# Kernel tuning notes

Measured on AMD Instinct MI355X. Metric: run time of the kernel, lower is better.

Reference implementation:

```python
import jax, jax.numpy as jnp
import numpy as np

B, H, S, DH = 1, 16, 4096, 64
SPARSITY = 0.1
NEG = -1e9


def setup_inputs() -> dict:
    key = jax.random.key(0)
    kq, kk, kv, kp, km = jax.random.split(key, 5)
    query = jax.random.normal(kq, (B, H, S, DH), dtype=jnp.float32)
    k_ = jax.random.normal(kk, (B, H, S, DH), dtype=jnp.float32)
    v_ = jax.random.normal(kv, (B, H, S, DH), dtype=jnp.float32)
    pat = jax.random.uniform(kp, (S, S)) < SPARSITY
    pat = pat | jnp.eye(S, dtype=bool)
    sparse_pattern = pat[None, None]  # [1,1,S,S]
    mask = jax.random.randint(km, (1, 1, 1, S), 0, 2, dtype=jnp.int32)
    return {"query": query, "key": k_, "value": v_,
            "sparse_pattern": sparse_pattern, "mask": mask}


def reference(query, key, value, sparse_pattern, mask):
    scale = 1.0 / jnp.sqrt(jnp.asarray(DH, dtype=query.dtype))
    # [B,H,S,S] attention scores
    scores = jnp.einsum('bhqd,bhkd->bhqk', query, key) * scale
    scores = jnp.where(sparse_pattern, scores, NEG)
    scores = jnp.where(mask == 0, NEG, scores)
    weights = jax.nn.softmax(scores, axis=-1)
    return jnp.einsum('bhqk,bhkd->bhqd', weights, value)
```

## Files before the change

### kernel.cpp

```cpp
#include <hip/hip_runtime.h>
#include <hip/hip_bf16.h>

#define S_LEN 4096
#define DHD   64
#define NH    16
#define NKT   64
#define KVB   64
#define WQ    32
#define NW    4
#define QB    (WQ * NW)
#define QSCALE 0.18033688011112042f
#define THRS   8.656170245333781f

#if __has_builtin(__builtin_amdgcn_exp2f)
#define EXP2(x) __builtin_amdgcn_exp2f(x)
#else
#define EXP2(x) exp2f(x)
#endif

typedef __bf16 bf16x8 __attribute__((ext_vector_type(8)));
typedef __bf16 bf16x4 __attribute__((ext_vector_type(4)));
typedef float  f32x16 __attribute__((ext_vector_type(16)));
typedef float  f32x4  __attribute__((ext_vector_type(4)));
typedef unsigned u32;
typedef unsigned u32x4v __attribute__((ext_vector_type(4)));
typedef unsigned long long u64;

__device__ __forceinline__ int swz(int row, int col) {
  return row * 64 + ((((col >> 3) ^ (row & 7)) << 3) | (col & 7));
}

__device__ __forceinline__ u32 pk(float a, float b) {
  __bf16 x = (__bf16)a, y = (__bf16)b;
  u32 lo = (u32)__builtin_bit_cast(unsigned short, x);
  u32 hi = (u32)__builtin_bit_cast(unsigned short, y);
  return lo | (hi << 16);
}

__device__ __forceinline__ void gload16(const void* g, void* l) {
  __builtin_amdgcn_global_load_lds((const __attribute__((address_space(1))) void*)g,
                                   (__attribute__((address_space(3))) void*)l, 16, 0, 0);
}

__device__ __forceinline__ void plswap(u32& x, u32& y) {
  asm("v_permlane32_swap_b32 %0, %1" : "+v"(x), "+v"(y));
}

union PAW { u32x4v w; bf16x8 h; };

template <int MODE>
__device__ __forceinline__ bool patget(const void* __restrict__ p, int q, int k) {
  const size_t idx = (size_t)q * S_LEN + k;
  if constexpr (MODE == 1) return ((const unsigned char*)p)[idx] != 0;
  else if constexpr (MODE == 0) return ((const int*)p)[idx] != 0;
  else return ((const float*)p)[idx] != 0.0f;
}

__global__ void __launch_bounds__(256, 2) attn32c(
    const float* __restrict__ Qg, const __bf16* __restrict__ Kc, const __bf16* __restrict__ Vc,
    const u64* __restrict__ packw,
    const int* __restrict__ cntp, float* __restrict__ out) {
  __shared__ __align__(16) __bf16 Kls[2][KVB * DHD];
  __shared__ __align__(16) __bf16 Vls[2][DHD * KVB];
  __shared__ float sfb[NW][WQ];

  const int gid = (blockIdx.x & 7) * 64 + (blockIdx.x >> 3);
  const int h = gid >> 5;
  const int q0 = (gid & 31) * QB;

  const int t = threadIdx.x, lane = t & 63, wv = t >> 6;
  const int l32 = lane & 31, hi = lane >> 5;
  const int qrow = q0 + wv * WQ + l32;
  const int nact = cntp[0];
  const int nt = (nact + 63) >> 6;

  bf16x8 aQ[4];
  {
    const float* qp = Qg + ((size_t)h * S_LEN + qrow) * DHD;
#pragma unroll
    for (int c = 0; c < 4; c++) {
      float4 x = *(const float4*)(qp + c * 16 + hi * 8);
      float4 y = *(const float4*)(qp + c * 16 + hi * 8 + 4);
      bf16x8 f;
      f[0] = (__bf16)(x.x * QSCALE); f[1] = (__bf16)(x.y * QSCALE);
      f[2] = (__bf16)(x.z * QSCALE); f[3] = (__bf16)(x.w * QSCALE);
      f[4] = (__bf16)(y.x * QSCALE); f[5] = (__bf16)(y.y * QSCALE);
      f[6] = (__bf16)(y.z * QSCALE); f[7] = (__bf16)(y.w * QSCALE);
      aQ[c] = f;
    }
  }
  bf16x8 onesf;
#pragma unroll
  for (int j = 0; j < 8; j++) onesf[j] = (__bf16)1.0f;

  const __bf16* Kb = Kc + (size_t)h * NKT * 4096;
  const __bf16* Vb = Vc + (size_t)h * NKT * 4096;

  auto stage = [&](int buf, int kt) {
    const __bf16* kbase = Kb + (size_t)kt * 4096;
    const __bf16* vbase = Vb + (size_t)kt * 4096;
#pragma unroll
    for (int i = 0; i < 2; i++) {
      const int j = wv * 2 + i;
      gload16(kbase + j * 512 + lane * 8, &Kls[buf][j * 512]);
      gload16(vbase + j * 512 + lane * 8, &Vls[buf][j * 512]);
    }
  };

  f32x16 Oc0, Oc1, Ol;
#pragma unroll
  for (int r = 0; r < 16; r++) { Oc0[r] = 0.f; Oc1[r] = 0.f; Ol[r] = 0.f; }
  float m_run = -__builtin_inff();
  const u64* prow = packw + qrow;

  u64 pw_cur = prow[0];
  u64 pw_nxt = 0;
  stage(0, 0);
  int cur = 0;

  for (int kt = 0; kt < nt; kt++) {
    if (kt + 1 < nt) {
      pw_nxt = prow[(size_t)(kt + 1) * S_LEN];
      stage(cur ^ 1, kt + 1);
      asm volatile("s_waitcnt vmcnt(5)" ::: "memory");
    } else {
      asm volatile("s_waitcnt vmcnt(0)" ::: "memory");
    }
    __builtin_amdgcn_s_barrier();
    __builtin_amdgcn_sched_barrier(0);

    const __bf16* Kl = Kls[cur];
    f32x16 p0, p1;
#pragma unroll
    for (int r = 0; r < 16; r++) { p0[r] = 0.f; p1[r] = 0.f; }
    __builtin_amdgcn_s_setprio(1);
#pragma unroll
    for (int c = 0; c < 4; c++) {
      const int g = (((2 * c + hi) ^ (l32 & 7)) << 3);
      const bf16x8 k0 = *(const bf16x8*)&Kl[l32 * 64 + g];
      const bf16x8 k1 = *(const bf16x8*)&Kl[(32 + l32) * 64 + g];
      p0 = __builtin_amdgcn_mfma_f32_32x32x16_bf16(k0, aQ[c], p0, 0, 0, 0);
      p1 = __builtin_amdgcn_mfma_f32_32x32x16_bf16(k1, aQ[c], p1, 0, 0, 0);
    }
    __builtin_amdgcn_s_setprio(0);

    float mx[16];
#pragma unroll
    for (int i = 0; i < 8; i++) mx[i] = fmaxf(p0[2 * i], p0[2 * i + 1]);
#pragma unroll
    for (int i = 0; i < 8; i++) mx[8 + i] = fmaxf(p1[2 * i], p1[2 * i + 1]);
#pragma unroll
    for (int s = 8; s >= 1; s >>= 1)
#pragma unroll
      for (int i = 0; i < s; i++) mx[i] = fmaxf(mx[i], mx[i + s]);
    const float pm = fmaxf(mx[0], __shfl_xor(mx[0], 32));

    if (!__all(pm <= m_run + THRS)) {
      const float mn = fmaxf(m_run, pm);
      const float sf = EXP2(m_run - mn);
      m_run = mn;
      if (lane < 32) sfb[wv][l32] = sf;
#pragma unroll
      for (int rq = 0; rq < 4; rq++) {
        const f32x4 s4 = *(const f32x4*)&sfb[wv][rq * 8 + 4 * hi];
#pragma unroll
        for (int rr = 0; rr < 4; rr++) {
          Oc0[rq * 4 + rr] *= s4[rr];
          Oc1[rq * 4 + rr] *= s4[rr];
          Ol[rq * 4 + rr]  *= s4[rr];
        }
      }
    }

    const u32 b0 = (u32)pw_cur, b1 = (u32)(pw_cur >> 32);
    const u32 w0 = hi ? ((b0 >> 4) | (b1 << 28)) : b0;
    const u32 w1 = hi ? (b1 >> 4) : b1;

#pragma unroll
    for (int r = 0; r < 16; r++) {
      const int sp = (r & 3) + 8 * (r >> 2);
      float e0 = EXP2(p0[r] - m_run);
      float e1 = EXP2(p1[r] - m_run);
      const int t0 = (int)(w0 << (31 - sp)) >> 31;
      const int t1 = (int)(w1 << (31 - sp)) >> 31;
      p0[r] = __uint_as_float(__float_as_uint(e0) & (u32)t0);
      p1[r] = __uint_as_float(__float_as_uint(e1) & (u32)t1);
    }

    const __bf16* Vl = Vls[cur];
    __builtin_amdgcn_s_setprio(1);
#pragma unroll
    for (int ks = 0; ks < 4; ks++) {
      const f32x16& ps = (ks < 2) ? p0 : p1;
      const int b = (ks & 1) * 8;
      u32 x0 = pk(ps[b + 0], ps[b + 1]), x1 = pk(ps[b + 2], ps[b + 3]);
      u32 y0 = pk(ps[b + 4], ps[b + 5]), y1 = pk(ps[b + 6], ps[b + 7]);
      plswap(x0, y0);
      plswap(x1, y1);
      PAW pa;
      pa.w = (u32x4v){x0, x1, y0, y1};
      const int g = (((2 * ks + hi) ^ (l32 & 7)) << 3);
      const bf16x8 v0 = *(const bf16x8*)&Vl[l32 * 64 + g];
      const bf16x8 v1 = *(const bf16x8*)&Vl[(32 + l32) * 64 + g];
      Oc0 = __builtin_amdgcn_mfma_f32_32x32x16_bf16(pa.h, v0, Oc0, 0, 0, 0);
      Oc1 = __builtin_amdgcn_mfma_f32_32x32x16_bf16(pa.h, v1, Oc1, 0, 0, 0);
      Ol  = __builtin_amdgcn_mfma_f32_32x32x16_bf16(pa.h, onesf, Ol, 0, 0, 0);
    }
    __builtin_amdgcn_s_setprio(0);

    __builtin_amdgcn_s_barrier();
    cur ^= 1;
    pw_cur = pw_nxt;
  }

  float* ob = out + ((size_t)h * S_LEN + q0 + wv * WQ) * DHD;
#pragma unroll
  for (int rq = 0; rq < 4; rq++) {
#pragma unroll
    for (int rr = 0; rr < 4; rr++) {
      const int r = rq * 4 + rr;
      const float linv = 1.0f / Ol[r];
      const int qq = rr + 8 * rq + 4 * hi;
      ob[(size_t)qq * DHD + l32]      = Oc0[r] * linv;
      ob[(size_t)qq * DHD + 32 + l32] = Oc1[r] * linv;
    }
  }
}

__global__ void prep0(const unsigned* __restrict__ p, int* __restrict__ flag,
                      const int* __restrict__ mask, int* __restrict__ idx,
                      int* __restrict__ cntp) {
  if (blockIdx.x == 0) {
    __shared__ unsigned red[256];
    const int t = threadIdx.x;
    unsigned acc = 0;
    for (int i = t; i < 16384; i += 256) {
      const unsigned w = p[i];
      if (w == 0x3F800000u) acc |= 2u;
      else if (w & 0xFFFFFF00u) acc |= 1u;
    }
    red[t] = acc;
    __syncthreads();
    if (t == 0) {
      unsigned a = 0;
      for (int i = 0; i < 256; i++) a |= red[i];
      flag[0] = (a & 2u) ? 2 : ((a & 1u) ? 1 : 0);
    }
  } else if (threadIdx.x < 64) {
    const int t = threadIdx.x;
    int cnt = 0;
    for (int j = 0; j < 64; j++) cnt += (mask[t * 64 + j] != 0);
    int inc = cnt;
    for (int d = 1; d < 64; d <<= 1) {
      const int v = __shfl_up(inc, d);
      if (t >= d) inc += v;
    }
    int pfx = inc - cnt;
    for (int j = 0; j < 64; j++) {
      const int k = t * 64 + j;
      if (mask[k] != 0) idx[pfx++] = k;
    }
    if (t == 63) cntp[0] = inc;
  }
}

__global__ void __launch_bounds__(256) prep1(
    const void* __restrict__ pat, const int* __restrict__ flagp,
    const int* __restrict__ idx, const int* __restrict__ cntp, u64* __restrict__ packw,
    const float* __restrict__ K, const float* __restrict__ V,
    __bf16* __restrict__ Kc, __bf16* __restrict__ Vc) {
  const int nact = cntp[0];
  const int t = threadIdx.x;
  if (blockIdx.x < S_LEN) {
    __shared__ __align__(16) unsigned rowbuf[4096];
    const int q = blockIdx.x;
    const int mode = flagp[0];
    if (mode == 1) {
      const uint4* src = (const uint4*)((const unsigned char*)pat + ((size_t)q << 12));
      ((uint4*)rowbuf)[t] = src[t];
    } else {
      const uint4* src = (const uint4*)((const unsigned*)pat + ((size_t)q << 12));
#pragma unroll
      for (int i = 0; i < 4; i++) ((uint4*)rowbuf)[t + 256 * i] = src[t + 256 * i];
    }
    __syncthreads();
    const unsigned char* rb = (const unsigned char*)rowbuf;
    for (int base = 0; base < nact; base += 256) {
      const int j = base + t;
      bool pb = false;
      if (j < nact) {
        const int k = idx[j];
        pb = (mode == 1) ? (rb[k] != 0) : (rowbuf[k] != 0);
      }
      const u64 b = __ballot(pb);
      if ((t & 63) == 0) packw[(size_t)(j >> 6) * S_LEN + q] = b;
    }
  } else {
    const int bb = blockIdx.x - S_LEN;
    const int kt = bb & 63, h = bb >> 6;
    if (kt >= ((nact + 63) >> 6)) return;
    __bf16* Kd = Kc + ((size_t)(h * NKT + kt)) * 4096;
    __bf16* Vd = Vc + ((size_t)(h * NKT + kt)) * 4096;
    const float* Kb = K + (size_t)h * S_LEN * DHD;
    const float* Vb = V + (size_t)h * S_LEN * DHD;
#pragma unroll
    for (int i = 0; i < 4; i++) {
      const int u = t + 256 * i;
      const int kk = u >> 4, d = (u & 15) * 4;
      const int kg = kt * 64 + kk;
      float4 v = {0.f, 0.f, 0.f, 0.f};
      if (kg < nact) v = *(const float4*)(Kb + (size_t)idx[kg] * DHD + d);
      bf16x4 b;
      b[0] = (__bf16)v.x; b[1] = (__bf16)v.y; b[2] = (__bf16)v.z; b[3] = (__bf16)v.w;
      *(bf16x4*)&Kd[swz(kk, d)] = b;
    }
#pragma unroll
    for (int i = 0; i < 2; i++) {
      const int u = t + 256 * i;
      const int kp = u & 31, d4 = u >> 5;
      const int g0 = kt * 64 + 2 * kp, g1 = g0 + 1;
      float4 a = {0.f, 0.f, 0.f, 0.f}, b = {0.f, 0.f, 0.f, 0.f};
      if (g0 < nact) a = *(const float4*)(Vb + (size_t)idx[g0] * DHD + d4 * 4);
      if (g1 < nact) b = *(const float4*)(Vb + (size_t)idx[g1] * DHD + d4 * 4);
      const float* A = reinterpret_cast<const float*>(&a);
      const float* B = reinterpret_cast<const float*>(&b);
#pragma unroll
      for (int j = 0; j < 4; j++) {
        *(u32*)&Vd[swz(d4 * 4 + j, 2 * kp)] = pk(A[j], B[j]);
      }
    }
  }
}

template <bool PACKED, int MODE>
__global__ void __launch_bounds__(256, 2) attn32(
    const float* __restrict__ Qg, const float* __restrict__ Kg, const float* __restrict__ Vg,
    const u64* __restrict__ packw, const void* __restrict__ pat, const int* __restrict__ mask,
    float* __restrict__ out) {
  __shared__ __align__(16) __bf16 Kls[2][KVB * DHD];
  __shared__ __align__(16) __bf16 Vls[2][DHD * KVB];
  __shared__ float sfb[NW][WQ];
  const int gid = (blockIdx.x & 7) * 64 + (blockIdx.x >> 3);
  const int h = gid >> 5;
  const int q0 = (gid & 31) * QB;
  const int t = threadIdx.x, lane = t & 63, wv = t >> 6;
  const int l32 = lane & 31, hi = lane >> 5;
  const int qrow = q0 + wv * WQ + l32;
  bf16x8 aQ[4];
  {
    const float* qp = Qg + ((size_t)h * S_LEN + qrow) * DHD;
#pragma unroll
    for (int c = 0; c < 4; c++) {
      float4 x = *(const float4*)(qp + c * 16 + hi * 8);
      float4 y = *(const float4*)(qp + c * 16 + hi * 8 + 4);
      bf16x8 f;
      f[0] = (__bf16)(x.x * QSCALE); f[1] = (__bf16)(x.y * QSCALE);
      f[2] = (__bf16)(x.z * QSCALE); f[3] = (__bf16)(x.w * QSCALE);
      f[4] = (__bf16)(y.x * QSCALE); f[5] = (__bf16)(y.y * QSCALE);
      f[6] = (__bf16)(y.z * QSCALE); f[7] = (__bf16)(y.w * QSCALE);
      aQ[c] = f;
    }
  }
  const float* Kb = Kg + (size_t)h * S_LEN * DHD;
  const float* Vb = Vg + (size_t)h * S_LEN * DHD;
  float4 kreg[4], vreg0[2], vreg1[2];
  auto issue_loads = [&](int kt) {
    const float* kbase = Kb + (size_t)kt * KVB * DHD;
    const float* vbase = Vb + (size_t)kt * KVB * DHD;
#pragma unroll
    for (int i = 0; i < 4; i++) {
      const int u = t + 256 * i;
      kreg[i] = *(const float4*)(kbase + (size_t)(u >> 4) * DHD + (u & 15) * 4);
    }
#pragma unroll
    for (int i = 0; i < 2; i++) {
      const int u = t + 256 * i;
      const int kp = u & 31, d4 = u >> 5;
      vreg0[i] = *(const float4*)(vbase + (size_t)(2 * kp) * DHD + d4 * 4);
      vreg1[i] = *(const float4*)(vbase + (size_t)(2 * kp + 1) * DHD + d4 * 4);
    }
  };
  auto write_tile = [&](int buf) {
    __bf16* Kd = Kls[buf];
    __bf16* Vd = Vls[buf];
#pragma unroll
    for (int i = 0; i < 4; i++) {
      const int u = t + 256 * i;
      const int kk = u >> 4, d = (u & 15) * 4;
      const float4 v = kreg[i];
      bf16x4 b;
      b[0] = (__bf16)v.x; b[1] = (__bf16)v.y; b[2] = (__bf16)v.z; b[3] = (__bf16)v.w;
      *(bf16x4*)&Kd[swz(kk, d)] = b;
    }
#pragma unroll
    for (int i = 0; i < 2; i++) {
      const int u = t + 256 * i;
      const int kp = u & 31, d4 = u >> 5;
      const float* A = reinterpret_cast<const float*>(&vreg0[i]);
      const float* B = reinterpret_cast<const float*>(&vreg1[i]);
#pragma unroll
      for (int j = 0; j < 4; j++) {
        *(u32*)&Vd[swz(d4 * 4 + j, 2 * kp)] = pk(A[j], B[j]);
      }
    }
  };
  f32x16 Oc0, Oc1;
#pragma unroll
  for (int r = 0; r < 16; r++) { Oc0[r] = 0.f; Oc1[r] = 0.f; }
  float m_run = -__builtin_inff(), l_run = 0.f;
  const u64* prow = PACKED ? (packw + qrow) : nullptr;
  issue_loads(0);
  write_tile(0);
  __syncthreads();
  int cur = 0;
  for (int kt = 0; kt < NKT; kt++) {
    if (kt + 1 < NKT) issue_loads(kt + 1);
    u64 pw;
    if constexpr (PACKED) {
      pw = prow[(size_t)kt * S_LEN];
    } else {
      pw = 0;
      for (int j = 0; j < 64; j++) {
        const bool pb = patget<MODE>(pat, qrow, kt * 64 + j) && (mask[kt * 64 + j] != 0);
        pw |= (u64)pb << j;
      }
    }
    const __bf16* Kl = Kls[cur];
    f32x16 p0, p1;
#pragma unroll
    for (int r = 0; r < 16; r++) { p0[r] = 0.f; p1[r] = 0.f; }
#pragma unroll
    for (int c = 0; c < 4; c++) {
      const int g = (((2 * c + hi) ^ (l32 & 7)) << 3);
      const bf16x8 k0 = *(const bf16x8*)&Kl[l32 * 64 + g];
      const bf16x8 k1 = *(const bf16x8*)&Kl[(32 + l32) * 64 + g];
      p0 = __builtin_amdgcn_mfma_f32_32x32x16_bf16(k0, aQ[c], p0, 0, 0, 0);
      p1 = __builtin_amdgcn_mfma_f32_32x32x16_bf16(k1, aQ[c], p1, 0, 0, 0);
    }
    float pm = p0[0];
#pragma unroll
    for (int r = 1; r < 16; r++) pm = fmaxf(pm, p0[r]);
#pragma unroll
    for (int r = 0; r < 16; r++) pm = fmaxf(pm, p1[r]);
    pm = fmaxf(pm, __shfl_xor(pm, 32));
    if (!__all(pm <= m_run + THRS)) {
      const float mn = fmaxf(m_run, pm);
      const float sf = EXP2(m_run - mn);
      m_run = mn;
      l_run *= sf;
      if (lane < 32) sfb[wv][l32] = sf;
#pragma unroll
      for (int rq = 0; rq < 4; rq++) {
        const f32x4 s4 = *(const f32x4*)&sfb[wv][rq * 8 + 4 * hi];
#pragma unroll
        for (int rr = 0; rr < 4; rr++) {
          Oc0[rq * 4 + rr] *= s4[rr];
          Oc1[rq * 4 + rr] *= s4[rr];
        }
      }
    }
    const u32 b0 = (u32)pw, b1 = (u32)(pw >> 32);
    const u32 w0 = hi ? ((b0 >> 4) | (b1 << 28)) : b0;
    const u32 w1 = hi ? (b1 >> 4) : b1;
    float ls = 0.f;
#pragma unroll
    for (int r = 0; r < 16; r++) {
      const int sp = (r & 3) + 8 * (r >> 2);
      float e0 = EXP2(p0[r] - m_run);
      float e1 = EXP2(p1[r] - m_run);
      const int t0 = (int)(w0 << (31 - sp)) >> 31;
      const int t1 = (int)(w1 << (31 - sp)) >> 31;
      e0 = __uint_as_float(__float_as_uint(e0) & (u32)t0);
      e1 = __uint_as_float(__float_as_uint(e1) & (u32)t1);
      p0[r] = e0; p1[r] = e1;
      ls += e0 + e1;
    }
    ls += __shfl_xor(ls, 32);
    l_run += ls;
    const __bf16* Vl = Vls[cur];
#pragma unroll
    for (int ks = 0; ks < 4; ks++) {
      const f32x16& ps = (ks < 2) ? p0 : p1;
      const int b = (ks & 1) * 8;
      u32 x0 = pk(ps[b + 0], ps[b + 1]), x1 = pk(ps[b + 2], ps[b + 3]);
      u32 y0 = pk(ps[b + 4], ps[b + 5]), y1 = pk(ps[b + 6], ps[b + 7]);
      plswap(x0, y0);
      plswap(x1, y1);
      PAW pa;
      pa.w = (u32x4v){x0, x1, y0, y1};
      const int g = (((2 * ks + hi) ^ (l32 & 7)) << 3);
      const bf16x8 v0 = *(const bf16x8*)&Vl[l32 * 64 + g];
      const bf16x8 v1 = *(const bf16x8*)&Vl[(32 + l32) * 64 + g];
      Oc0 = __builtin_amdgcn_mfma_f32_32x32x16_bf16(pa.h, v0, Oc0, 0, 0, 0);
      Oc1 = __builtin_amdgcn_mfma_f32_32x32x16_bf16(pa.h, v1, Oc1, 0, 0, 0);
    }
    if (kt + 1 < NKT) write_tile(cur ^ 1);
    __syncthreads();
    cur ^= 1;
  }
  const float linv = 1.0f / l_run;
  if (lane < 32) sfb[wv][l32] = linv;
  __syncthreads();
  float* ob = out + ((size_t)h * S_LEN + q0 + wv * WQ) * DHD;
#pragma unroll
  for (int rq = 0; rq < 4; rq++) {
    const f32x4 s4 = *(const f32x4*)&sfb[wv][rq * 8 + 4 * hi];
#pragma unroll
    for (int rr = 0; rr < 4; rr++) {
      const int r = rq * 4 + rr;
      const int qq = rr + 8 * rq + 4 * hi;
      ob[(size_t)qq * DHD + l32]      = Oc0[r] * s4[rr];
      ob[(size_t)qq * DHD + 32 + l32] = Oc1[r] * s4[rr];
    }
  }
}

__global__ void detect_kernel(const unsigned* __restrict__ p, int* __restrict__ flag) {
  __shared__ unsigned red[256];
  const int t = threadIdx.x;
  unsigned acc = 0;
  for (int i = t; i < 16384; i += 256) {
    const unsigned w = p[i];
    if (w == 0x3F800000u) acc |= 2u;
    else if (w & 0xFFFFFF00u) acc |= 1u;
  }
  red[t] = acc;
  __syncthreads();
  if (t == 0) {
    unsigned a = 0;
    for (int i = 0; i < 256; i++) a |= red[i];
    flag[0] = (a & 2u) ? 2 : ((a & 1u) ? 1 : 0);
  }
}

__global__ void pack_mask_kernel(const int* __restrict__ mask, u64* __restrict__ maskw) {
  const int w = threadIdx.x;
  u64 m = 0;
  for (int j = 0; j < 64; j++) m |= (u64)(mask[(w << 6) + j] != 0) << j;
  maskw[w] = m;
}

__global__ void pack_pat_kernel(const void* __restrict__ pat, const u64* __restrict__ maskw,
                                u64* __restrict__ packw, const int* __restrict__ flagp) {
  const int gid = blockIdx.x * 256 + threadIdx.x;
  const int q = gid >> 6, w = gid & 63;
  const int mode = flagp[0];
  u64 bits = 0;
  if (mode == 1) {
    const u64* p = (const u64*)((const unsigned char*)pat + ((size_t)q << 12) + (w << 6));
#pragma unroll
    for (int c = 0; c < 8; c++) {
      u64 v = p[c];
      v |= v >> 4; v |= v >> 2; v |= v >> 1;
      v &= 0x0101010101010101ull;
      bits |= ((v * 0x0102040810204080ull) >> 56) << (c * 8);
    }
  } else if (mode == 0) {
    const int4* p = (const int4*)((const int*)pat + ((size_t)q << 12) + ((size_t)w << 6));
#pragma unroll
    for (int c = 0; c < 16; c++) {
      const int4 x = p[c];
      bits |= (u64)(x.x != 0) << (c * 4);
      bits |= (u64)(x.y != 0) << (c * 4 + 1);
      bits |= (u64)(x.z != 0) << (c * 4 + 2);
      bits |= (u64)(x.w != 0) << (c * 4 + 3);
    }
  } else {
    const float4* p = (const float4*)((const float*)pat + ((size_t)q << 12) + ((size_t)w << 6));
#pragma unroll
    for (int c = 0; c < 16; c++) {
      const float4 x = p[c];
      bits |= (u64)(x.x != 0.0f) << (c * 4);
      bits |= (u64)(x.y != 0.0f) << (c * 4 + 1);
      bits |= (u64)(x.z != 0.0f) << (c * 4 + 2);
      bits |= (u64)(x.w != 0.0f) << (c * 4 + 3);
    }
  }
  packw[(size_t)w * S_LEN + q] = bits & maskw[w];
}

extern "C" void kernel_launch(void* const* d_in, const int* in_sizes, int n_in,
                              void* d_out, int out_size, void* d_ws, size_t ws_size,
                              hipStream_t stream) {
  (void)in_sizes; (void)n_in; (void)out_size;
  const float* Q  = (const float*)d_in[0];
  const float* K  = (const float*)d_in[1];
  const float* V  = (const float*)d_in[2];
  const void* pat = d_in[3];
  const int* mask = (const int*)d_in[4];
  float* out      = (float*)d_out;

  const size_t FLAG_OFF  = 0;
  const size_t CNT_OFF   = 256;
  const size_t IDX_OFF   = 4096;
  const size_t MASKW_OFF = 24576;
  const size_t PACKW_OFF = 32768;
  const size_t KC_OFF    = PACKW_OFF + (size_t)S_LEN * NKT * 8;
  const size_t VC_OFF    = KC_OFF + (size_t)NH * NKT * 4096 * 2;
  const size_t NEED_FULL = VC_OFF + (size_t)NH * NKT * 4096 * 2;
  const size_t NEED_MID  = PACKW_OFF + (size_t)S_LEN * NKT * 8;

  const dim3 grid(32 * NH, 1);

  if (ws_size >= NEED_FULL) {
    int* flag  = (int*)((char*)d_ws + FLAG_OFF);
    int* cnt   = (int*)((char*)d_ws + CNT_OFF);
    int* idx   = (int*)((char*)d_ws + IDX_OFF);
    u64* packw = (u64*)((char*)d_ws + PACKW_OFF);
    __bf16* Kc = (__bf16*)((char*)d_ws + KC_OFF);
    __bf16* Vc = (__bf16*)((char*)d_ws + VC_OFF);
    prep0<<<2, 256, 0, stream>>>((const unsigned*)pat, flag, mask, idx, cnt);
    prep1<<<S_LEN + NKT * NH, 256, 0, stream>>>(pat, flag, idx, cnt, packw, K, V, Kc, Vc);
    attn32c<<<grid, 256, 0, stream>>>(Q, Kc, Vc, packw, cnt, out);
  } else if (ws_size >= NEED_MID) {
    int* flag  = (int*)((char*)d_ws + FLAG_OFF);
    u64* maskw = (u64*)((char*)d_ws + MASKW_OFF);
    u64* packw = (u64*)((char*)d_ws + PACKW_OFF);
    detect_kernel<<<1, 256, 0, stream>>>((const unsigned*)pat, flag);
    pack_mask_kernel<<<1, 64, 0, stream>>>(mask, maskw);
    pack_pat_kernel<<<(S_LEN * 64) / 256, 256, 0, stream>>>(pat, maskw, packw, flag);
    attn32<true, 0><<<grid, 256, 0, stream>>>(Q, K, V, packw, pat, mask, out);
  } else {
    attn32<false, 1><<<grid, 256, 0, stream>>>(Q, K, V, nullptr, pat, mask, out);
  }
}
```

Baseline: 101.6 us.

## Merge prep kernels into one and process two KV tiles per iteration

The two preprocessing launches are merged into a single kernel that recomputes the mask prefix sum, index list and pattern-type detection inside every block. The attention kernel now counts active keys itself from the mask instead of reading a count from a prior kernel. Its main loop handles two compacted KV tiles per iteration with a four-slot LDS ring, halving barriers and online-softmax rescale checks. The cost is redundant per-block prefix scans and type detection, doubled LDS for K/V, more live registers, and padding the tile count to an even number.

```diff
diff --git a/kernel.cpp b/kernel.cpp
--- a/kernel.cpp
+++ b/kernel.cpp
@@ -26,6 +26,8 @@
 typedef unsigned u32x4v __attribute__((ext_vector_type(4)));
 typedef unsigned long long u64;
 
+#define MFMA32 __builtin_amdgcn_mfma_f32_32x32x16_bf16
+
 __device__ __forceinline__ int swz(int row, int col) {
   return row * 64 + ((((col >> 3) ^ (row & 7)) << 3) | (col & 7));
 }
@@ -59,10 +61,11 @@
 __global__ void __launch_bounds__(256, 2) attn32c(
     const float* __restrict__ Qg, const __bf16* __restrict__ Kc, const __bf16* __restrict__ Vc,
     const u64* __restrict__ packw,
-    const int* __restrict__ cntp, float* __restrict__ out) {
-  __shared__ __align__(16) __bf16 Kls[2][KVB * DHD];
-  __shared__ __align__(16) __bf16 Vls[2][DHD * KVB];
+    const int* __restrict__ mask, float* __restrict__ out) {
+  __shared__ __align__(16) __bf16 Kls[4][KVB * DHD];
+  __shared__ __align__(16) __bf16 Vls[4][DHD * KVB];
   __shared__ float sfb[NW][WQ];
+  __shared__ int msum[NW];
 
   const int gid = (blockIdx.x & 7) * 64 + (blockIdx.x >> 3);
   const int h = gid >> 5;
@@ -71,86 +74,111 @@
   const int t = threadIdx.x, lane = t & 63, wv = t >> 6;
   const int l32 = lane & 31, hi = lane >> 5;
   const int qrow = q0 + wv * WQ + l32;
-  const int nact = cntp[0];
-  const int nt = (nact + 63) >> 6;
+
+  int c = 0;
+#pragma unroll
+  for (int j = 0; j < 16; j++) c += (mask[t * 16 + j] != 0);
+#pragma unroll
+  for (int d = 1; d < 64; d <<= 1) c += __shfl_xor(c, d);
+  if (lane == 0) msum[wv] = c;
 
   bf16x8 aQ[4];
   {
     const float* qp = Qg + ((size_t)h * S_LEN + qrow) * DHD;
 #pragma unroll
-    for (int c = 0; c < 4; c++) {
-      float4 x = *(const float4*)(qp + c * 16 + hi * 8);
-      float4 y = *(const float4*)(qp + c * 16 + hi * 8 + 4);
+    for (int cc = 0; cc < 4; cc++) {
+      float4 x = *(const float4*)(qp + cc * 16 + hi * 8);
+      float4 y = *(const float4*)(qp + cc * 16 + hi * 8 + 4);
       bf16x8 f;
       f[0] = (__bf16)(x.x * QSCALE); f[1] = (__bf16)(x.y * QSCALE);
       f[2] = (__bf16)(x.z * QSCALE); f[3] = (__bf16)(x.w * QSCALE);
       f[4] = (__bf16)(y.x * QSCALE); f[5] = (__bf16)(y.y * QSCALE);
       f[6] = (__bf16)(y.z * QSCALE); f[7] = (__bf16)(y.w * QSCALE);
-      aQ[c] = f;
+      aQ[cc] = f;
     }
   }
   bf16x8 onesf;
 #pragma unroll
   for (int j = 0; j < 8; j++) onesf[j] = (__bf16)1.0f;
+  f32x16 zv;
+#pragma unroll
+  for (int r = 0; r < 16; r++) zv[r] = 0.f;
+
+  __syncthreads();
+  const int nact = msum[0] + msum[1] + msum[2] + msum[3];
+  const int nt = (nact + 63) >> 6;
+  const int np = ((nt + 1) & ~1) >> 1;
 
   const __bf16* Kb = Kc + (size_t)h * NKT * 4096;
   const __bf16* Vb = Vc + (size_t)h * NKT * 4096;
 
-  auto stage = [&](int buf, int kt) {
+  auto stage = [&](int slot, int kt) {
     const __bf16* kbase = Kb + (size_t)kt * 4096;
     const __bf16* vbase = Vb + (size_t)kt * 4096;
 #pragma unroll
     for (int i = 0; i < 2; i++) {
       const int j = wv * 2 + i;
-      gload16(kbase + j * 512 + lane * 8, &Kls[buf][j * 512]);
-      gload16(vbase + j * 512 + lane * 8, &Vls[buf][j * 512]);
+      gload16(kbase + j * 512 + lane * 8, &Kls[slot][j * 512]);
+      gload16(vbase + j * 512 + lane * 8, &Vls[slot][j * 512]);
     }
   };
 
-  f32x16 Oc0, Oc1, Ol;
-#pragma unroll
-  for (int r = 0; r < 16; r++) { Oc0[r] = 0.f; Oc1[r] = 0.f; Ol[r] = 0.f; }
+  f32x16 Oc0 = zv, Oc1 = zv, Ol = zv;
   float m_run = -__builtin_inff();
   const u64* prow = packw + qrow;
 
-  u64 pw_cur = prow[0];
-  u64 pw_nxt = 0;
+  __builtin_amdgcn_sched_barrier(0);
+  u64 pwA = prow[0];
+  u64 pwB = prow[(size_t)1 * S_LEN];
   stage(0, 0);
-  int cur = 0;
-
-  for (int kt = 0; kt < nt; kt++) {
-    if (kt + 1 < nt) {
-      pw_nxt = prow[(size_t)(kt + 1) * S_LEN];
-      stage(cur ^ 1, kt + 1);
-      asm volatile("s_waitcnt vmcnt(5)" ::: "memory");
+  stage(1, 1);
+
+  for (int it = 0; it < np; it++) {
+    const int buf = (it & 1) << 1;
+    u64 pwA_n = 0, pwB_n = 0;
+    if (it + 1 < np) {
+      pwA_n = prow[(size_t)(2 * it + 2) * S_LEN];
+      pwB_n = prow[(size_t)(2 * it + 3) * S_LEN];
+      stage(buf ^ 2, 2 * it + 2);
+      stage((buf ^ 2) + 1, 2 * it + 3);
+      asm volatile("s_waitcnt vmcnt(10)" ::: "memory");
     } else {
       asm volatile("s_waitcnt vmcnt(0)" ::: "memory");
     }
     __builtin_amdgcn_s_barrier();
     __builtin_amdgcn_sched_barrier(0);
 
-    const __bf16* Kl = Kls[cur];
-    f32x16 p0, p1;
-#pragma unroll
-    for (int r = 0; r < 16; r++) { p0[r] = 0.f; p1[r] = 0.f; }
+    const __bf16* KlA = Kls[buf];
+    const __bf16* KlB = Kls[buf + 1];
+    const __bf16* VlA = Vls[buf];
+    const __bf16* VlB = Vls[buf + 1];
+
+    f32x16 pA0, pA1, pB0, pB1;
     __builtin_amdgcn_s_setprio(1);
 #pragma unroll
-    for (int c = 0; c < 4; c++) {
-      const int g = (((2 * c + hi) ^ (l32 & 7)) << 3);
-      const bf16x8 k0 = *(const bf16x8*)&Kl[l32 * 64 + g];
-      const bf16x8 k1 = *(const bf16x8*)&Kl[(32 + l32) * 64 + g];
-      p0 = __builtin_amdgcn_mfma_f32_32x32x16_bf16(k0, aQ[c], p0, 0, 0, 0);
-      p1 = __builtin_amdgcn_mfma_f32_32x32x16_bf16(k1, aQ[c], p1, 0, 0, 0);
+    for (int cc = 0; cc < 4; cc++) {
+      const int g = (((2 * cc + hi) ^ (l32 & 7)) << 3);
+      const bf16x8 kA0 = *(const bf16x8*)&KlA[l32 * 64 + g];
+      const bf16x8 kA1 = *(const bf16x8*)&KlA[(32 + l32) * 64 + g];
+      const bf16x8 kB0 = *(const bf16x8*)&KlB[l32 * 64 + g];
+      const bf16x8 kB1 = *(const bf16x8*)&KlB[(32 + l32) * 64 + g];
+      pA0 = MFMA32(kA0, aQ[cc], cc ? pA0 : zv, 0, 0, 0);
+      pA1 = MFMA32(kA1, aQ[cc], cc ? pA1 : zv, 0, 0, 0);
+      pB0 = MFMA32(kB0, aQ[cc], cc ? pB0 : zv, 0, 0, 0);
+      pB1 = MFMA32(kB1, aQ[cc], cc ? pB1 : zv, 0, 0, 0);
     }
     __builtin_amdgcn_s_setprio(0);
 
-    float mx[16];
-#pragma unroll
-    for (int i = 0; i < 8; i++) mx[i] = fmaxf(p0[2 * i], p0[2 * i + 1]);
-#pragma unroll
-    for (int i = 0; i < 8; i++) mx[8 + i] = fmaxf(p1[2 * i], p1[2 * i + 1]);
-#pragma unroll
-    for (int s = 8; s >= 1; s >>= 1)
+    float mx[32];
+#pragma unroll
+    for (int i = 0; i < 8; i++) {
+      mx[i]      = fmaxf(pA0[2 * i], pA0[2 * i + 1]);
+      mx[8 + i]  = fmaxf(pA1[2 * i], pA1[2 * i + 1]);
+      mx[16 + i] = fmaxf(pB0[2 * i], pB0[2 * i + 1]);
+      mx[24 + i] = fmaxf(pB1[2 * i], pB1[2 * i + 1]);
+    }
+#pragma unroll
+    for (int s = 16; s >= 1; s >>= 1)
 #pragma unroll
       for (int i = 0; i < s; i++) mx[i] = fmaxf(mx[i], mx[i + s]);
     const float pm = fmaxf(mx[0], __shfl_xor(mx[0], 32));
@@ -172,26 +200,34 @@
       }
     }
 
-    const u32 b0 = (u32)pw_cur, b1 = (u32)(pw_cur >> 32);
-    const u32 w0 = hi ? ((b0 >> 4) | (b1 << 28)) : b0;
-    const u32 w1 = hi ? (b1 >> 4) : b1;
+    const u32 a0b = (u32)pwA, a1b = (u32)(pwA >> 32);
+    const u32 wA0 = hi ? ((a0b >> 4) | (a1b << 28)) : a0b;
+    const u32 wA1 = hi ? (a1b >> 4) : a1b;
+    const u32 b0b = (u32)pwB, b1b = (u32)(pwB >> 32);
+    const u32 wB0 = hi ? ((b0b >> 4) | (b1b << 28)) : b0b;
+    const u32 wB1 = hi ? (b1b >> 4) : b1b;
 
 #pragma unroll
     for (int r = 0; r < 16; r++) {
       const int sp = (r & 3) + 8 * (r >> 2);
-      float e0 = EXP2(p0[r] - m_run);
-      float e1 = EXP2(p1[r] - m_run);
-      const int t0 = (int)(w0 << (31 - sp)) >> 31;
-      const int t1 = (int)(w1 << (31 - sp)) >> 31;
-      p0[r] = __uint_as_float(__float_as_uint(e0) & (u32)t0);
-      p1[r] = __uint_as_float(__float_as_uint(e1) & (u32)t1);
-    }
-
-    const __bf16* Vl = Vls[cur];
+      float eA0 = EXP2(pA0[r] - m_run);
+      float eA1 = EXP2(pA1[r] - m_run);
+      float eB0 = EXP2(pB0[r] - m_run);
+      float eB1 = EXP2(pB1[r] - m_run);
+      const int tA0 = (int)(wA0 << (31 - sp)) >> 31;
+      const int tA1 = (int)(wA1 << (31 - sp)) >> 31;
+      const int tB0 = (int)(wB0 << (31 - sp)) >> 31;
+      const int tB1 = (int)(wB1 << (31 - sp)) >> 31;
+      pA0[r] = __uint_as_float(__float_as_uint(eA0) & (u32)tA0);
+      pA1[r] = __uint_as_float(__float_as_uint(eA1) & (u32)tA1);
+      pB0[r] = __uint_as_float(__float_as_uint(eB0) & (u32)tB0);
+      pB1[r] = __uint_as_float(__float_as_uint(eB1) & (u32)tB1);
+    }
+
     __builtin_amdgcn_s_setprio(1);
 #pragma unroll
     for (int ks = 0; ks < 4; ks++) {
-      const f32x16& ps = (ks < 2) ? p0 : p1;
+      const f32x16& ps = (ks < 2) ? pA0 : pA1;
       const int b = (ks & 1) * 8;
       u32 x0 = pk(ps[b + 0], ps[b + 1]), x1 = pk(ps[b + 2], ps[b + 3]);
       u32 y0 = pk(ps[b + 4], ps[b + 5]), y1 = pk(ps[b + 6], ps[b + 7]);
@@ -200,17 +236,34 @@
       PAW pa;
       pa.w = (u32x4v){x0, x1, y0, y1};
       const int g = (((2 * ks + hi) ^ (l32 & 7)) << 3);
-      const bf16x8 v0 = *(const bf16x8*)&Vl[l32 * 64 + g];
-      const bf16x8 v1 = *(const bf16x8*)&Vl[(32 + l32) * 64 + g];
-      Oc0 = __builtin_amdgcn_mfma_f32_32x32x16_bf16(pa.h, v0, Oc0, 0, 0, 0);
-      Oc1 = __builtin_amdgcn_mfma_f32_32x32x16_bf16(pa.h, v1, Oc1, 0, 0, 0);
-      Ol  = __builtin_amdgcn_mfma_f32_32x32x16_bf16(pa.h, onesf, Ol, 0, 0, 0);
+      const bf16x8 v0 = *(const bf16x8*)&VlA[l32 * 64 + g];
+      const bf16x8 v1 = *(const bf16x8*)&VlA[(32 + l32) * 64 + g];
+      Oc0 = MFMA32(pa.h, v0, Oc0, 0, 0, 0);
+      Oc1 = MFMA32(pa.h, v1, Oc1, 0, 0, 0);
+      Ol  = MFMA32(pa.h, onesf, Ol, 0, 0, 0);
+    }
+#pragma unroll
+    for (int ks = 0; ks < 4; ks++) {
+      const f32x16& ps = (ks < 2) ? pB0 : pB1;
+      const int b = (ks & 1) * 8;
+      u32 x0 = pk(ps[b + 0], ps[b + 1]), x1 = pk(ps[b + 2], ps[b + 3]);
+      u32 y0 = pk(ps[b + 4], ps[b + 5]), y1 = pk(ps[b + 6], ps[b + 7]);
+      plswap(x0, y0);
+      plswap(x1, y1);
+      PAW pa;
+      pa.w = (u32x4v){x0, x1, y0, y1};
+      const int g = (((2 * ks + hi) ^ (l32 & 7)) << 3);
+      const bf16x8 v0 = *(const bf16x8*)&VlB[l32 * 64 + g];
+      const bf16x8 v1 = *(const bf16x8*)&VlB[(32 + l32) * 64 + g];
+      Oc0 = MFMA32(pa.h, v0, Oc0, 0, 0, 0);
+      Oc1 = MFMA32(pa.h, v1, Oc1, 0, 0, 0);
+      Ol  = MFMA32(pa.h, onesf, Ol, 0, 0, 0);
     }
     __builtin_amdgcn_s_setprio(0);
 
     __builtin_amdgcn_s_barrier();
-    cur ^= 1;
-    pw_cur = pw_nxt;
+    pwA = pwA_n;
+    pwB = pwB_n;
   }
 
   float* ob = out + ((size_t)h * S_LEN + q0 + wv * WQ) * DHD;
@@ -227,69 +280,67 @@
   }
 }
 
-__global__ void prep0(const unsigned* __restrict__ p, int* __restrict__ flag,
-                      const int* __restrict__ mask, int* __restrict__ idx,
-                      int* __restrict__ cntp) {
-  if (blockIdx.x == 0) {
-    __shared__ unsigned red[256];
-    const int t = threadIdx.x;
+__global__ void __launch_bounds__(256) prep_all(
+    const unsigned* __restrict__ pat32, const int* __restrict__ mask,
+    const float* __restrict__ K, const float* __restrict__ V,
+    u64* __restrict__ packw, __bf16* __restrict__ Kc, __bf16* __restrict__ Vc) {
+  __shared__ int idxs[S_LEN];
+  __shared__ int red8[8];
+  __shared__ __align__(16) unsigned rowbuf[4096];
+  const int t = threadIdx.x, lane = t & 63, wv = t >> 6;
+
+  unsigned mb = 0;
+#pragma unroll
+  for (int j = 0; j < 16; j++) mb |= (unsigned)(mask[t * 16 + j] != 0) << j;
+  const int cnt = __builtin_popcount(mb);
+  int inc = cnt;
+  for (int d = 1; d < 64; d <<= 1) {
+    const int v = __shfl_up(inc, d);
+    if (lane >= d) inc += v;
+  }
+  if (lane == 63) red8[wv] = inc;
+  __syncthreads();
+  int base = 0;
+  for (int w = 0; w < wv; w++) base += red8[w];
+  const int nact = red8[0] + red8[1] + red8[2] + red8[3];
+  int pfx = base + inc - cnt;
+#pragma unroll
+  for (int j = 0; j < 16; j++)
+    if ((mb >> j) & 1) idxs[pfx++] = t * 16 + j;
+  __syncthreads();
+  const int nt = (nact + 63) >> 6;
+  const int nte = (nt + 1) & ~1;
+
+  if (blockIdx.x < S_LEN) {
+    const int q = blockIdx.x;
     unsigned acc = 0;
-    for (int i = t; i < 16384; i += 256) {
-      const unsigned w = p[i];
+    for (int i = t; i < 4096; i += 256) {
+      const unsigned w = pat32[i];
       if (w == 0x3F800000u) acc |= 2u;
       else if (w & 0xFFFFFF00u) acc |= 1u;
     }
-    red[t] = acc;
+    for (int d = 1; d < 64; d <<= 1) acc |= (unsigned)__shfl_xor((int)acc, d);
+    if (lane == 0) red8[4 + wv] = (int)acc;
     __syncthreads();
-    if (t == 0) {
-      unsigned a = 0;
-      for (int i = 0; i < 256; i++) a |= red[i];
-      flag[0] = (a & 2u) ? 2 : ((a & 1u) ? 1 : 0);
-    }
-  } else if (threadIdx.x < 64) {
-    const int t = threadIdx.x;
-    int cnt = 0;
-    for (int j = 0; j < 64; j++) cnt += (mask[t * 64 + j] != 0);
-    int inc = cnt;
-    for (int d = 1; d < 64; d <<= 1) {
-      const int v = __shfl_up(inc, d);
-      if (t >= d) inc += v;
-    }
-    int pfx = inc - cnt;
-    for (int j = 0; j < 64; j++) {
-      const int k = t * 64 + j;
-      if (mask[k] != 0) idx[pfx++] = k;
-    }
-    if (t == 63) cntp[0] = inc;
-  }
-}
-
-__global__ void __launch_bounds__(256) prep1(
-    const void* __restrict__ pat, const int* __restrict__ flagp,
-    const int* __restrict__ idx, const int* __restrict__ cntp, u64* __restrict__ packw,
-    const float* __restrict__ K, const float* __restrict__ V,
-    __bf16* __restrict__ Kc, __bf16* __restrict__ Vc) {
-  const int nact = cntp[0];
-  const int t = threadIdx.x;
-  if (blockIdx.x < S_LEN) {
-    __shared__ __align__(16) unsigned rowbuf[4096];
-    const int q = blockIdx.x;
-    const int mode = flagp[0];
+    acc = (unsigned)(red8[4] | red8[5] | red8[6] | red8[7]);
+    const int mode = (acc & 2u) ? 2 : ((acc & 1u) ? 1 : 0);
+
     if (mode == 1) {
-      const uint4* src = (const uint4*)((const unsigned char*)pat + ((size_t)q << 12));
+      const uint4* src = (const uint4*)((const unsigned char*)pat32 + ((size_t)q << 12));
       ((uint4*)rowbuf)[t] = src[t];
     } else {
-      const uint4* src = (const uint4*)((const unsigned*)pat + ((size_t)q << 12));
+      const uint4* src = (const uint4*)(pat32 + ((size_t)q << 12));
 #pragma unroll
       for (int i = 0; i < 4; i++) ((uint4*)rowbuf)[t + 256 * i] = src[t + 256 * i];
     }
     __syncthreads();
     const unsigned char* rb = (const unsigned char*)rowbuf;
-    for (int base = 0; base < nact; base += 256) {
-      const int j = base + t;
+    const int nkw = nte * 64;
+    for (int bs = 0; bs < nkw; bs += 256) {
+      const int j = bs + t;
       bool pb = false;
       if (j < nact) {
-        const int k = idx[j];
+        const int k = idxs[j];
         pb = (mode == 1) ? (rb[k] != 0) : (rowbuf[k] != 0);
       }
       const u64 b = __ballot(pb);
@@ -298,7 +349,7 @@
   } else {
     const int bb = blockIdx.x - S_LEN;
     const int kt = bb & 63, h = bb >> 6;
-    if (kt >= ((nact + 63) >> 6)) return;
+    if (kt >= nte) return;
     __bf16* Kd = Kc + ((size_t)(h * NKT + kt)) * 4096;
     __bf16* Vd = Vc + ((size_t)(h * NKT + kt)) * 4096;
     const float* Kb = K + (size_t)h * S_LEN * DHD;
@@ -309,7 +360,7 @@
       const int kk = u >> 4, d = (u & 15) * 4;
       const int kg = kt * 64 + kk;
       float4 v = {0.f, 0.f, 0.f, 0.f};
-      if (kg < nact) v = *(const float4*)(Kb + (size_t)idx[kg] * DHD + d);
+      if (kg < nact) v = *(const float4*)(Kb + (size_t)idxs[kg] * DHD + d);
       bf16x4 b;
       b[0] = (__bf16)v.x; b[1] = (__bf16)v.y; b[2] = (__bf16)v.z; b[3] = (__bf16)v.w;
       *(bf16x4*)&Kd[swz(kk, d)] = b;
@@ -320,8 +371,8 @@
       const int kp = u & 31, d4 = u >> 5;
       const int g0 = kt * 64 + 2 * kp, g1 = g0 + 1;
       float4 a = {0.f, 0.f, 0.f, 0.f}, b = {0.f, 0.f, 0.f, 0.f};
-      if (g0 < nact) a = *(const float4*)(Vb + (size_t)idx[g0] * DHD + d4 * 4);
-      if (g1 < nact) b = *(const float4*)(Vb + (size_t)idx[g1] * DHD + d4 * 4);
+      if (g0 < nact) a = *(const float4*)(Vb + (size_t)idxs[g0] * DHD + d4 * 4);
+      if (g1 < nact) b = *(const float4*)(Vb + (size_t)idxs[g1] * DHD + d4 * 4);
       const float* A = reinterpret_cast<const float*>(&a);
       const float* B = reinterpret_cast<const float*>(&b);
 #pragma unroll
@@ -350,15 +401,15 @@
   {
     const float* qp = Qg + ((size_t)h * S_LEN + qrow) * DHD;
 #pragma unroll
-    for (int c = 0; c < 4; c++) {
-      float4 x = *(const float4*)(qp + c * 16 + hi * 8);
-      float4 y = *(const float4*)(qp + c * 16 + hi * 8 + 4);
+    for (int cc = 0; cc < 4; cc++) {
+      float4 x = *(const float4*)(qp + cc * 16 + hi * 8);
+      float4 y = *(const float4*)(qp + cc * 16 + hi * 8 + 4);
       bf16x8 f;
       f[0] = (__bf16)(x.x * QSCALE); f[1] = (__bf16)(x.y * QSCALE);
       f[2] = (__bf16)(x.z * QSCALE); f[3] = (__bf16)(x.w * QSCALE);
       f[4] = (__bf16)(y.x * QSCALE); f[5] = (__bf16)(y.y * QSCALE);
       f[6] = (__bf16)(y.z * QSCALE); f[7] = (__bf16)(y.w * QSCALE);
-      aQ[c] = f;
+      aQ[cc] = f;
     }
   }
   const float* Kb = Kg + (size_t)h * S_LEN * DHD;
@@ -430,12 +481,12 @@
 #pragma unroll
     for (int r = 0; r < 16; r++) { p0[r] = 0.f; p1[r] = 0.f; }
 #pragma unroll
-    for (int c = 0; c < 4; c++) {
-      const int g = (((2 * c + hi) ^ (l32 & 7)) << 3);
+    for (int cc = 0; cc < 4; cc++) {
+      const int g = (((2 * cc + hi) ^ (l32 & 7)) << 3);
       const bf16x8 k0 = *(const bf16x8*)&Kl[l32 * 64 + g];
       const bf16x8 k1 = *(const bf16x8*)&Kl[(32 + l32) * 64 + g];
-      p0 = __builtin_amdgcn_mfma_f32_32x32x16_bf16(k0, aQ[c], p0, 0, 0, 0);
-      p1 = __builtin_amdgcn_mfma_f32_32x32x16_bf16(k1, aQ[c], p1, 0, 0, 0);
+      p0 = MFMA32(k0, aQ[cc], p0, 0, 0, 0);
+      p1 = MFMA32(k1, aQ[cc], p1, 0, 0, 0);
     }
     float pm = p0[0];
 #pragma unroll
@@ -491,8 +542,8 @@
       const int g = (((2 * ks + hi) ^ (l32 & 7)) << 3);
       const bf16x8 v0 = *(const bf16x8*)&Vl[l32 * 64 + g];
       const bf16x8 v1 = *(const bf16x8*)&Vl[(32 + l32) * 64 + g];
-      Oc0 = __builtin_amdgcn_mfma_f32_32x32x16_bf16(pa.h, v0, Oc0, 0, 0, 0);
-      Oc1 = __builtin_amdgcn_mfma_f32_32x32x16_bf16(pa.h, v1, Oc1, 0, 0, 0);
+      Oc0 = MFMA32(pa.h, v0, Oc0, 0, 0, 0);
+      Oc1 = MFMA32(pa.h, v1, Oc1, 0, 0, 0);
     }
     if (kt + 1 < NKT) write_tile(cur ^ 1);
     __syncthreads();
@@ -591,8 +642,6 @@
   float* out      = (float*)d_out;
 
   const size_t FLAG_OFF  = 0;
-  const size_t CNT_OFF   = 256;
-  const size_t IDX_OFF   = 4096;
   const size_t MASKW_OFF = 24576;
   const size_t PACKW_OFF = 32768;
   const size_t KC_OFF    = PACKW_OFF + (size_t)S_LEN * NKT * 8;
@@ -603,15 +652,12 @@
   const dim3 grid(32 * NH, 1);
 
   if (ws_size >= NEED_FULL) {
-    int* flag  = (int*)((char*)d_ws + FLAG_OFF);
-    int* cnt   = (int*)((char*)d_ws + CNT_OFF);
-    int* idx   = (int*)((char*)d_ws + IDX_OFF);
     u64* packw = (u64*)((char*)d_ws + PACKW_OFF);
     __bf16* Kc = (__bf16*)((char*)d_ws + KC_OFF);
     __bf16* Vc = (__bf16*)((char*)d_ws + VC_OFF);
-    prep0<<<2, 256, 0, stream>>>((const unsigned*)pat, flag, mask, idx, cnt);
-    prep1<<<S_LEN + NKT * NH, 256, 0, stream>>>(pat, flag, idx, cnt, packw, K, V, Kc, Vc);
-    attn32c<<<grid, 256, 0, stream>>>(Q, Kc, Vc, packw, cnt, out);
+    prep_all<<<S_LEN + NKT * NH, 256, 0, stream>>>((const unsigned*)pat, mask, K, V,
+                                                   packw, Kc, Vc);
+    attn32c<<<grid, 256, 0, stream>>>(Q, Kc, Vc, packw, mask, out);
   } else if (ws_size >= NEED_MID) {
     int* flag  = (int*)((char*)d_ws + FLAG_OFF);
     u64* maskw = (u64*)((char*)d_ws + MASKW_OFF);
```

Measured after the change: 95.40 us. 6.1% less time.
